# Performance work log

Measured on AMD Instinct MI355X. Metric: run time of the kernel, lower is better.

Reference implementation:

```python
import jax, jax.numpy as jnp
import numpy as np

K, D = 1024, 256
B, H, W = 16, 64, 64


def setup_inputs() -> dict:
    key = jax.random.key(0)
    k1, k2 = jax.random.split(key)
    z_e_x = jax.random.normal(k1, (B, D, H, W), dtype=jnp.float32)
    # nn.Embedding weight initialized uniform(-1/K, 1/K)
    embedding = jax.random.uniform(k2, (K, D), dtype=jnp.float32,
                                   minval=-1.0 / K, maxval=1.0 / K)
    return {"z_e_x": z_e_x, "embedding": embedding}


def reference(z_e_x, embedding):
    # permute(0,2,3,1): [B,D,H,W] -> [B,H,W,D]
    z = jnp.transpose(z_e_x, (0, 2, 3, 1))
    flat = z.reshape(-1, z.shape[-1])  # [N, D], N = B*H*W
    # squared L2 distances: ||z||^2 - 2 z.e + ||e||^2  -> [N, K]
    dists = (jnp.sum(flat * flat, axis=1, keepdims=True)
             - 2.0 * flat @ embedding.T
             + jnp.sum(embedding * embedding, axis=1))
    indices = jnp.argmin(dists, axis=1)  # [N]
    # vq() returns latents with the spatial shape [B, H, W]
    return indices.reshape(z.shape[:-1]).astype(jnp.int32)
```

## Files before the change

### kernel.cpp

```cpp
#include <hip/hip_runtime.h>


#define D_DIM  256
#define K_DIM  1024
#define HW     4096
#define N_TOT  65536
#define NSPLIT 4
#define KSPL   (K_DIM / NSPLIT)
#define KT     64
#define NKT    (KSPL / KT)
#define F32MAX 3.402823466e38f


__global__ void ee_kernel(const float* __restrict__ e, float* __restrict__ ee) {
#pragma clang fp contract(off)
    int k = blockIdx.x * blockDim.x + threadIdx.x;
    if (k >= K_DIM) return;
    const float* row = e + (size_t)k * D_DIM;
    float total = 0.0f;
    #pragma unroll
    for (int h = 0; h < 2; ++h) {
        const float* a = row + h * 128;
        float r[8];
        #pragma unroll
        for (int j = 0; j < 8; ++j) { float v = a[j]; r[j] = v * v; }
        #pragma unroll
        for (int i = 8; i < 128; i += 8) {
            #pragma unroll
            for (int j = 0; j < 8; ++j) { float v = a[i + j]; r[j] = r[j] + v * v; }
        }
        float s = ((r[0] + r[1]) + (r[2] + r[3])) + ((r[4] + r[5]) + (r[6] + r[7]));
        total = (h == 0) ? s : (total + s);
    }
    ee[k] = total;
}

__global__ void a_kernel(const float* __restrict__ z, float* __restrict__ A) {
#pragma clang fp contract(off)
    int n = blockIdx.x * blockDim.x + threadIdx.x;
    int b  = n >> 12;
    int hw = n & (HW - 1);
    const float* base = z + (size_t)b * D_DIM * HW + hw;
    float total = 0.0f;
    #pragma unroll
    for (int h = 0; h < 2; ++h) {
        float r[8];
        #pragma unroll
        for (int j = 0; j < 8; ++j) {
            float v = base[(size_t)(h * 128 + j) * HW];
            r[j] = v * v;
        }
        #pragma unroll
        for (int i = 8; i < 128; i += 8) {
            #pragma unroll
            for (int j = 0; j < 8; ++j) {
                float v = base[(size_t)(h * 128 + i + j) * HW];
                r[j] = r[j] + v * v;
            }
        }
        float s = ((r[0] + r[1]) + (r[2] + r[3])) + ((r[4] + r[5]) + (r[6] + r[7]));
        total = (h == 0) ? s : (total + s);
    }
    A[n] = total;
}


__global__ void et_kernel(const float* __restrict__ e, float* __restrict__ eT) {
    int k = blockIdx.x;
    int d = threadIdx.x;
    eT[(size_t)d * K_DIM + k] = 2.0f * e[(size_t)k * D_DIM + d];
}


__launch_bounds__(256, 4)
__global__ void vq_partial(const float* __restrict__ z, const float* __restrict__ eT,
                           const float* __restrict__ A, const float* __restrict__ ee,
                           float* __restrict__ pv, int* __restrict__ pk) {
#pragma clang fp contract(off)
    const int tid  = threadIdx.x;
    const int s    = blockIdx.x & (NSPLIT - 1);
    const int slab = blockIdx.x >> 2;
    const int n    = slab * 256 + tid;
    const int b    = n >> 12;
    const int hw   = n & (HW - 1);
    const float* __restrict__ zp = z + (size_t)b * D_DIM * HW + hw;
    const int kb0 = s * KSPL;

    const float An = A[n];
    float bestv = F32MAX;
    int   bestk = 0;

    float za[8], zb[8];
    #pragma unroll
    for (int i = 0; i < 8; ++i) za[i] = zp[(size_t)i * HW];

    #pragma unroll 1
    for (int kt = 0; kt < NKT; ++kt) {
        const int kbase = kb0 + kt * KT;
        float acc[KT];
        #pragma unroll
        for (int j = 0; j < KT; ++j) acc[j] = 0.0f;

        #pragma unroll 1
        for (int it = 0; it < 16; ++it) {
            const int base = it * 16;
            #pragma unroll
            for (int i = 0; i < 8; ++i)
                zb[i] = zp[(size_t)((base + 8 + i) & (D_DIM - 1)) * HW];
            #pragma unroll
            for (int dd = 0; dd < 8; ++dd) {
                const float zv = za[dd];
                const float* __restrict__ er = eT + (size_t)(base + dd) * K_DIM + kbase;
                #pragma unroll
                for (int j = 0; j < KT; ++j)
                    acc[j] = fmaf(zv, er[j], acc[j]);
            }
            #pragma unroll
            for (int i = 0; i < 8; ++i)
                za[i] = zp[(size_t)((base + 16 + i) & (D_DIM - 1)) * HW];
            #pragma unroll
            for (int dd = 0; dd < 8; ++dd) {
                const float zv = zb[dd];
                const float* __restrict__ er = eT + (size_t)(base + 8 + dd) * K_DIM + kbase;
                #pragma unroll
                for (int j = 0; j < KT; ++j)
                    acc[j] = fmaf(zv, er[j], acc[j]);
            }
        }

        #pragma unroll
        for (int j = 0; j < KT; ++j) {
            const float dist = (An - acc[j]) + ee[kbase + j];
            if (dist < bestv) { bestv = dist; bestk = kbase + j; }
        }
    }

    pv[(size_t)s * N_TOT + n] = bestv;
    pk[(size_t)s * N_TOT + n] = bestk;
}


__global__ void combine_kernel(const float* __restrict__ pv, const int* __restrict__ pk,
                               int* __restrict__ out) {
    int n = blockIdx.x * blockDim.x + threadIdx.x;
    float bv = pv[n];
    int   bk = pk[n];
    #pragma unroll
    for (int s2 = 1; s2 < NSPLIT; ++s2) {
        float v = pv[(size_t)s2 * N_TOT + n];
        int   k = pk[(size_t)s2 * N_TOT + n];
        if (v < bv) { bv = v; bk = k; }
    }
    out[n] = bk;
}

extern "C" void kernel_launch(void* const* d_in, const int* in_sizes, int n_in,
                              void* d_out, int out_size, void* d_ws, size_t ws_size,
                              hipStream_t stream) {
    const float* z   = (const float*)d_in[0];
    const float* emb = (const float*)d_in[1];
    int* out = (int*)d_out;

    float* wsA  = (float*)d_ws;
    float* wsEE = wsA + N_TOT;
    float* wsET = wsEE + K_DIM;
    float* wsPV = wsET + (size_t)D_DIM * K_DIM;
    int*   wsPK = (int*)(wsPV + (size_t)NSPLIT * N_TOT);

    et_kernel<<<K_DIM, 256, 0, stream>>>(emb, wsET);
    ee_kernel<<<K_DIM / 256, 256, 0, stream>>>(emb, wsEE);
    a_kernel<<<N_TOT / 256, 256, 0, stream>>>(z, wsA);
    vq_partial<<<N_TOT / 256 * NSPLIT, 256, 0, stream>>>(z, wsET, wsA, wsEE, wsPV, wsPK);
    combine_kernel<<<N_TOT / 256, 256, 0, stream>>>(wsPV, wsPK, out);
}
```

Baseline: 512.7 us.

## Split K range 16 ways with atomicMin packed argmin and tiled transpose

Splits the codebook into 16 slices, one 64-wide accumulator tile per block, so each block does a single pass over D instead of looping over several K tiles. This gives more blocks and raises the launch-bounds occupancy hint from 4 to 5. Per-slice results are merged with a 64-bit atomicMin on an order-preserving float key packed with the index, replacing the separate partial arrays and combine kernel. This adds a memset and an unpack kernel. The embedding transpose now goes through a shared-memory tile so both its reads and writes are coalesced. The cost is that z is re-read 16 times instead of 4, plus atomic traffic.

```diff
diff --git a/kernel.cpp b/kernel.cpp
--- a/kernel.cpp
+++ b/kernel.cpp
@@ -5,10 +5,8 @@
 #define K_DIM  1024
 #define HW     4096
 #define N_TOT  65536
-#define NSPLIT 4
+#define NSPLIT 16
 #define KSPL   (K_DIM / NSPLIT)
-#define KT     64
-#define NKT    (KSPL / KT)
 #define F32MAX 3.402823466e38f
 
 
@@ -66,92 +64,91 @@
 
 
 __global__ void et_kernel(const float* __restrict__ e, float* __restrict__ eT) {
-    int k = blockIdx.x;
-    int d = threadIdx.x;
-    eT[(size_t)d * K_DIM + k] = 2.0f * e[(size_t)k * D_DIM + d];
+    __shared__ float t[32][33];
+    const int k0 = blockIdx.x * 32;
+    const int d0 = blockIdx.y * 32;
+    const int tx = threadIdx.x;
+    const int ty = threadIdx.y;
+    #pragma unroll
+    for (int i = 0; i < 32; i += 8)
+        t[ty + i][tx] = 2.0f * e[(size_t)(k0 + ty + i) * D_DIM + d0 + tx];
+    __syncthreads();
+    #pragma unroll
+    for (int i = 0; i < 32; i += 8)
+        eT[(size_t)(d0 + ty + i) * K_DIM + k0 + tx] = t[tx][ty + i];
 }
 
 
-__launch_bounds__(256, 4)
+__launch_bounds__(256, 5)
 __global__ void vq_partial(const float* __restrict__ z, const float* __restrict__ eT,
                            const float* __restrict__ A, const float* __restrict__ ee,
-                           float* __restrict__ pv, int* __restrict__ pk) {
+                           unsigned long long* __restrict__ packed) {
 #pragma clang fp contract(off)
     const int tid  = threadIdx.x;
     const int s    = blockIdx.x & (NSPLIT - 1);
-    const int slab = blockIdx.x >> 2;
+    const int slab = blockIdx.x >> 4;
     const int n    = slab * 256 + tid;
     const int b    = n >> 12;
     const int hw   = n & (HW - 1);
     const float* __restrict__ zp = z + (size_t)b * D_DIM * HW + hw;
-    const int kb0 = s * KSPL;
+    const int kbase = s * KSPL;
 
     const float An = A[n];
-    float bestv = F32MAX;
-    int   bestk = 0;
+
+    float acc[KSPL];
+    #pragma unroll
+    for (int j = 0; j < KSPL; ++j) acc[j] = 0.0f;
 
     float za[8], zb[8];
     #pragma unroll
     for (int i = 0; i < 8; ++i) za[i] = zp[(size_t)i * HW];
 
     #pragma unroll 1
-    for (int kt = 0; kt < NKT; ++kt) {
-        const int kbase = kb0 + kt * KT;
-        float acc[KT];
+    for (int it = 0; it < 16; ++it) {
+        const int base = it * 16;
         #pragma unroll
-        for (int j = 0; j < KT; ++j) acc[j] = 0.0f;
-
-        #pragma unroll 1
-        for (int it = 0; it < 16; ++it) {
-            const int base = it * 16;
+        for (int i = 0; i < 8; ++i)
+            zb[i] = zp[(size_t)((base + 8 + i) & (D_DIM - 1)) * HW];
+        #pragma unroll
+        for (int dd = 0; dd < 8; ++dd) {
+            const float zv = za[dd];
+            const float* __restrict__ er = eT + (size_t)(base + dd) * K_DIM + kbase;
             #pragma unroll
-            for (int i = 0; i < 8; ++i)
-                zb[i] = zp[(size_t)((base + 8 + i) & (D_DIM - 1)) * HW];
+            for (int j = 0; j < KSPL; ++j)
+                acc[j] = fmaf(zv, er[j], acc[j]);
+        }
+        #pragma unroll
+        for (int i = 0; i < 8; ++i)
+            za[i] = zp[(size_t)((base + 16 + i) & (D_DIM - 1)) * HW];
+        #pragma unroll
+        for (int dd = 0; dd < 8; ++dd) {
+            const float zv = zb[dd];
+            const float* __restrict__ er = eT + (size_t)(base + 8 + dd) * K_DIM + kbase;
             #pragma unroll
-            for (int dd = 0; dd < 8; ++dd) {
-                const float zv = za[dd];
-                const float* __restrict__ er = eT + (size_t)(base + dd) * K_DIM + kbase;
-                #pragma unroll
-                for (int j = 0; j < KT; ++j)
-                    acc[j] = fmaf(zv, er[j], acc[j]);
-            }
-            #pragma unroll
-            for (int i = 0; i < 8; ++i)
-                za[i] = zp[(size_t)((base + 16 + i) & (D_DIM - 1)) * HW];
-            #pragma unroll
-            for (int dd = 0; dd < 8; ++dd) {
-                const float zv = zb[dd];
-                const float* __restrict__ er = eT + (size_t)(base + 8 + dd) * K_DIM + kbase;
-                #pragma unroll
-                for (int j = 0; j < KT; ++j)
-                    acc[j] = fmaf(zv, er[j], acc[j]);
-            }
-        }
-
-        #pragma unroll
-        for (int j = 0; j < KT; ++j) {
-            const float dist = (An - acc[j]) + ee[kbase + j];
-            if (dist < bestv) { bestv = dist; bestk = kbase + j; }
+            for (int j = 0; j < KSPL; ++j)
+                acc[j] = fmaf(zv, er[j], acc[j]);
         }
     }
 
-    pv[(size_t)s * N_TOT + n] = bestv;
-    pk[(size_t)s * N_TOT + n] = bestk;
+    float bestv = F32MAX;
+    int   bestk = 0;
+    #pragma unroll
+    for (int j = 0; j < KSPL; ++j) {
+        const float dist = (An - acc[j]) + ee[kbase + j];
+        if (dist < bestv) { bestv = dist; bestk = kbase + j; }
+    }
+
+    unsigned int vb = __float_as_uint(bestv);
+    vb = (vb & 0x80000000u) ? ~vb : (vb | 0x80000000u);
+    const unsigned long long key =
+        ((unsigned long long)vb << 32) | (unsigned int)bestk;
+    atomicMin(&packed[n], key);
 }
 
-
-__global__ void combine_kernel(const float* __restrict__ pv, const int* __restrict__ pk,
-                               int* __restrict__ out) {
+__global__ void unpack_kernel(const unsigned long long* __restrict__ packed,
+                              int* __restrict__ out) {
     int n = blockIdx.x * blockDim.x + threadIdx.x;
-    float bv = pv[n];
-    int   bk = pk[n];
-    #pragma unroll
-    for (int s2 = 1; s2 < NSPLIT; ++s2) {
-        float v = pv[(size_t)s2 * N_TOT + n];
-        int   k = pk[(size_t)s2 * N_TOT + n];
-        if (v < bv) { bv = v; bk = k; }
-    }
-    out[n] = bk;
+    out[n] = (int)(packed[n] & 0xFFFFFFFFull);
 }
 
 extern "C" void kernel_launch(void* const* d_in, const int* in_sizes, int n_in,
@@ -164,12 +161,15 @@
     float* wsA  = (float*)d_ws;
     float* wsEE = wsA + N_TOT;
     float* wsET = wsEE + K_DIM;
-    float* wsPV = wsET + (size_t)D_DIM * K_DIM;
-    int*   wsPK = (int*)(wsPV + (size_t)NSPLIT * N_TOT);
+    unsigned long long* wsPacked =
+        (unsigned long long*)(wsET + (size_t)D_DIM * K_DIM);
 
-    et_kernel<<<K_DIM, 256, 0, stream>>>(emb, wsET);
+    hipMemsetAsync(wsPacked, 0xFF, (size_t)N_TOT * sizeof(unsigned long long),
+                   stream);
+    et_kernel<<<dim3(K_DIM / 32, D_DIM / 32), dim3(32, 8), 0, stream>>>(emb, wsET);
     ee_kernel<<<K_DIM / 256, 256, 0, stream>>>(emb, wsEE);
     a_kernel<<<N_TOT / 256, 256, 0, stream>>>(z, wsA);
-    vq_partial<<<N_TOT / 256 * NSPLIT, 256, 0, stream>>>(z, wsET, wsA, wsEE, wsPV, wsPK);
-    combine_kernel<<<N_TOT / 256, 256, 0, stream>>>(wsPV, wsPK, out);
+    vq_partial<<<N_TOT / 256 * NSPLIT, 256, 0, stream>>>(z, wsET, wsA, wsEE,
+                                                         wsPacked);
+    unpack_kernel<<<N_TOT / 256, 256, 0, stream>>>(wsPacked, out);
 }
```

Result: slower. 1.187 ms (+131.5%).
